# Performance work log

Measured on AMD Instinct MI355X. Metric: run time of the kernel, lower is better.

## Reference

```python
import jax, jax.numpy as jnp
import numpy as np

N_NODES = 50000
N_EDGES = 1600000
N_GRAPHS = 128
DIM_IN = 128
DIM_SELF = 16


def setup_inputs() -> dict:
    key = jax.random.key(0)
    ks = jax.random.split(key, 12)
    feat = jax.random.normal(ks[0], (N_NODES, DIM_IN), dtype=jnp.float32)
    self_feat = jax.random.normal(ks[1], (N_GRAPHS, DIM_SELF), dtype=jnp.float32)
    src = jax.random.randint(ks[2], (N_EDGES,), 0, N_NODES)
    dst = jax.random.randint(ks[3], (N_EDGES,), 0, N_NODES)
    graph_id = jnp.sort(jax.random.randint(ks[4], (N_NODES,), 0, N_GRAPHS))
    def lin(k, fan_in, fan_out):
        bound = 1.0 / np.sqrt(fan_in)
        return jax.random.uniform(k, (fan_in, fan_out), dtype=jnp.float32, minval=-bound, maxval=bound)
    W1 = lin(ks[5], DIM_IN, 100)
    b1 = jnp.zeros((100,), jnp.float32)
    W2 = lin(ks[6], 100, 20)
    b2 = jnp.zeros((20,), jnp.float32)
    Wf1 = lin(ks[7], 20 + DIM_SELF, 10)
    bf1 = jnp.zeros((10,), jnp.float32)
    Wf2 = lin(ks[8], 10, 1)
    bf2 = jnp.zeros((1,), jnp.float32)
    return {"feat": feat, "self_feat": self_feat, "src": src, "dst": dst,
            "graph_id": graph_id, "W1": W1, "b1": b1, "W2": W2, "b2": b2,
            "Wf1": Wf1, "bf1": bf1, "Wf2": Wf2, "bf2": bf2}


def _gcn_layer(h, src, dst, deg, W, b):
    # copy_u gather over edges + mean segment reduce over dst, then linear apply
    msg_sum = jax.ops.segment_sum(h[src], dst, num_segments=h.shape[0])  # [N, d]
    mean = msg_sum / jnp.maximum(deg, 1.0)[:, None]
    # DGL update_all leaves zero-in-degree nodes with their prior feature
    h_agg = jnp.where((deg > 0)[:, None], mean, h)
    return h_agg @ W + b


def reference(feat, self_feat, src, dst, graph_id, W1, b1, W2, b2, Wf1, bf1, Wf2, bf2):
    n = feat.shape[0]
    deg = jax.ops.segment_sum(jnp.ones((src.shape[0],), feat.dtype), dst, num_segments=n)
    h = jax.nn.relu(_gcn_layer(feat, src, dst, deg, W1, b1))   # [N,100]
    h = jax.nn.relu(_gcn_layer(h, src, dst, deg, W2, b2))      # [N,20]
    # dgl.mean_nodes: per-graph mean of node features
    g_sum = jax.ops.segment_sum(h, graph_id, num_segments=N_GRAPHS)  # [G,20]
    g_cnt = jax.ops.segment_sum(jnp.ones((n,), h.dtype), graph_id, num_segments=N_GRAPHS)
    hg = g_sum / jnp.maximum(g_cnt, 1.0)[:, None]
    fused = jnp.concatenate([hg, self_feat], axis=1)           # [G, 20+dim_self]
    out = jax.nn.relu(fused @ Wf1 + bf1) @ Wf2 + bf2           # [G, dim_out]
    return out
```

## Files before the change

### kernel.cpp

```cpp
#include <hip/hip_runtime.h>

constexpr int NN = 50000;
constexpr int NE = 1600000;
constexpr int NG = 128;
constexpr int BSTRIDE = 96;

constexpr int FILL_PASSES = 8;
constexpr int NODES_PER_PASS = 6250;
constexpr int BLOCKS_PER_PASS = (NE + 255) / 256;

constexpr int A1_NODES = 16;
constexpr int A1_BLOCKS = NN / A1_NODES;
constexpr int A2_BLOCKS = NN / 16;

#define OFF_CNT      0
#define OFF_GSUM     200000
#define OFF_GCNT     210240
#define ZERO_BYTES   210752
#define OFF_ADJ      210752
#define OFF_X1F      9810816
#define OFF_X2B      16210816

typedef float v2f __attribute__((ext_vector_type(2)));

__device__ __forceinline__ unsigned short f2bf(float x) {
    unsigned int v = __float_as_uint(x);
    return (unsigned short)((v + 0x7FFFu + ((v >> 16) & 1u)) >> 16);
}
__device__ __forceinline__ float bflo(unsigned int u) { return __uint_as_float(u << 16); }
__device__ __forceinline__ float bfhi(unsigned int u) { return __uint_as_float(u & 0xFFFF0000u); }

__global__ void k_fill(const int* __restrict__ src, const int* __restrict__ dst,
                       int* __restrict__ cnt, unsigned short* __restrict__ adj) {
    const int pass = blockIdx.x & 7;
    const int chunk = blockIdx.x >> 3;
    const int i = chunk * 256 + threadIdx.x;
    if (i >= NE) return;
    const int d = dst[i];
    const int lo = pass * NODES_PER_PASS;
    if (d >= lo && d < lo + NODES_PER_PASS) {
        const int p = atomicAdd(&cnt[d], 1);
        if (p < BSTRIDE) adj[d * BSTRIDE + p] = (unsigned short)src[i];
    }
}

__global__ __launch_bounds__(256) void k_gemm1(const float4* __restrict__ feat4,
                                               const float* __restrict__ W1,
                                               unsigned int* __restrict__ X1f) {
    const int t = threadIdx.x;
    if (t >= 250) return;
    const int cg = t % 25;
    const int nq = t / 25;
    const int node0 = blockIdx.x * 40 + nq * 4;
    const int col0 = cg * 4;

    float acc[4][4];
#pragma unroll
    for (int i = 0; i < 4; ++i)
#pragma unroll
        for (int j = 0; j < 4; ++j) acc[i][j] = 0.f;

    for (int k4 = 0; k4 < 32; ++k4) {
        float4 f[4];
#pragma unroll
        for (int i = 0; i < 4; ++i) f[i] = feat4[(node0 + i) * 32 + k4];
        float4 wr[4];
#pragma unroll
        for (int kk = 0; kk < 4; ++kk)
            wr[kk] = *(const float4*)(W1 + (k4 * 4 + kk) * 100 + col0);
#pragma unroll
        for (int kk = 0; kk < 4; ++kk) {
#pragma unroll
            for (int i = 0; i < 4; ++i) {
                const float fv = (kk == 0) ? f[i].x
                               : (kk == 1) ? f[i].y
                               : (kk == 2) ? f[i].z : f[i].w;
                acc[i][0] += fv * wr[kk].x;
                acc[i][1] += fv * wr[kk].y;
                acc[i][2] += fv * wr[kk].z;
                acc[i][3] += fv * wr[kk].w;
            }
        }
    }
#pragma unroll
    for (int i = 0; i < 4; ++i) {
        int u = 0;
        u = __builtin_amdgcn_cvt_pk_fp8_f32(acc[i][0], acc[i][1], u, false);
        u = __builtin_amdgcn_cvt_pk_fp8_f32(acc[i][2], acc[i][3], u, true);
        X1f[(node0 + i) * 32 + cg] = (unsigned int)u;
        if (cg == 24) {
#pragma unroll
            for (int z = 25; z < 32; ++z) X1f[(node0 + i) * 32 + z] = 0u;
        }
    }
}

__global__ __launch_bounds__(256) void k_agg1g2(
        const uint4* __restrict__ X1u, const int* __restrict__ cnt,
        const unsigned short* __restrict__ adj, const float* __restrict__ b1,
        const float* __restrict__ W2, unsigned int* __restrict__ X2b) {
    __shared__ float hl[A1_NODES * 100];
    __shared__ float w2s[100 * 20];
    const int t = threadIdx.x;
    const int node0 = blockIdx.x * A1_NODES;
    for (int i = t; i < 2000; i += 256) w2s[i] = W2[i];

    const int nl   = t >> 4;
    const int l    = t & 15;
    const int q    = l & 7;
    const int half = l >> 3;
    const int node = node0 + nl;
    const int d = cnt[node];
    const unsigned short* ab = adj + node * BSTRIDE;
    float a[16];
#pragma unroll
    for (int j = 0; j < 16; ++j) a[j] = 0.f;

#define ACC4(UU, B) { v2f l_ = __builtin_amdgcn_cvt_pk_f32_fp8((int)(UU), false); \
                      v2f h_ = __builtin_amdgcn_cvt_pk_f32_fp8((int)(UU), true);  \
                      a[B+0] += l_.x; a[B+1] += l_.y; a[B+2] += h_.x; a[B+3] += h_.y; }
#define SET4(UU, B) { v2f l_ = __builtin_amdgcn_cvt_pk_f32_fp8((int)(UU), false); \
                      v2f h_ = __builtin_amdgcn_cvt_pk_f32_fp8((int)(UU), true);  \
                      a[B+0] = l_.x; a[B+1] = l_.y; a[B+2] = h_.x; a[B+3] = h_.y; }

    if (q < 7) {
        if (d == 0) {
            if (half == 0) {
                const uint4 u = X1u[node * 8 + q];
                SET4(u.x, 0) SET4(u.y, 4) SET4(u.z, 8) SET4(u.w, 12)
            }
        } else {
            const int i0 = half ? (d >> 1) : 0;
            const int i1 = half ? d : (d >> 1);
            for (int i = i0; i < i1; ++i) {
                const int s = (int)ab[i];
                const uint4 u = X1u[s * 8 + q];
                ACC4(u.x, 0) ACC4(u.y, 4) ACC4(u.z, 8) ACC4(u.w, 12)
            }
        }
    }
#undef ACC4
#undef SET4
#pragma unroll
    for (int j = 0; j < 16; ++j) a[j] += __shfl_xor(a[j], 8);

    if (half == 0 && q < 7) {
        if (d > 0) {
            const float inv = 1.f / (float)d;
#pragma unroll
            for (int j = 0; j < 16; ++j) a[j] *= inv;
        }
        const int col0 = 16 * q;
        float* hrow = hl + nl * 100 + col0;
        const int nc = (q < 6) ? 16 : 4;
#pragma unroll 4
        for (int j = 0; j < nc; ++j)
            hrow[j] = fmaxf(a[j] + b1[col0 + j], 0.f);
    }
    __syncthreads();

    const int j = t & 15;
    unsigned int o = 0u;
    if (j < 10) {
        const float* h = hl + nl * 100;
        float a0 = 0.f, a1 = 0.f;
#pragma unroll 5
        for (int k = 0; k < 100; ++k) {
            const float hv = h[k];
            a0 += hv * w2s[k * 20 + 2 * j];
            a1 += hv * w2s[k * 20 + 2 * j + 1];
        }
        o = (unsigned int)f2bf(a0) | ((unsigned int)f2bf(a1) << 16);
    }
    X2b[node * 16 + j] = o;
}

__global__ __launch_bounds__(256) void k_agg2(const uint2* __restrict__ X2v,
                                              const int* __restrict__ cnt,
                                              const unsigned short* __restrict__ adj,
                                              const float* __restrict__ b2,
                                              const int* __restrict__ graph_id,
                                              float* __restrict__ g_sum,
                                              float* __restrict__ g_cnt) {
    __shared__ float lsum[NG * 20];
    __shared__ float lcnt[NG];
    const int t = threadIdx.x;
    for (int i = t; i < NG * 20; i += 256) lsum[i] = 0.f;
    if (t < NG) lcnt[t] = 0.f;
    __syncthreads();

    const int nl   = t >> 4;
    const int l    = t & 15;
    const int q    = l & 7;
    const int half = l >> 3;
    const int node = blockIdx.x * 16 + nl;
    const int d = cnt[node];
    const unsigned short* ab = adj + node * BSTRIDE;
    float ax = 0.f, ay = 0.f, az = 0.f, aw = 0.f;
    if (q < 5) {
        if (d == 0) {
            if (half == 0) {
                const uint2 u = X2v[node * 8 + q];
                ax = bflo(u.x); ay = bfhi(u.x);
                az = bflo(u.y); aw = bfhi(u.y);
            }
        } else {
            const int i0 = half ? (d >> 1) : 0;
            const int i1 = half ? d : (d >> 1);
            for (int i = i0; i < i1; ++i) {
                const int s = (int)ab[i];
                const uint2 u = X2v[s * 8 + q];
                ax += bflo(u.x); ay += bfhi(u.x);
                az += bflo(u.y); aw += bfhi(u.y);
            }
        }
    }
    ax += __shfl_xor(ax, 8);
    ay += __shfl_xor(ay, 8);
    az += __shfl_xor(az, 8);
    aw += __shfl_xor(aw, 8);

    if (half == 0 && q < 5) {
        if (d > 0) {
            const float inv = 1.f / (float)d;
            ax *= inv; ay *= inv; az *= inv; aw *= inv;
        }
        const int col0 = 4 * q;
        const float hx = fmaxf(ax + b2[col0 + 0], 0.f);
        const float hy = fmaxf(ay + b2[col0 + 1], 0.f);
        const float hz = fmaxf(az + b2[col0 + 2], 0.f);
        const float hw = fmaxf(aw + b2[col0 + 3], 0.f);
        const int g = graph_id[node];
        atomicAdd(&lsum[g * 20 + col0 + 0], hx);
        atomicAdd(&lsum[g * 20 + col0 + 1], hy);
        atomicAdd(&lsum[g * 20 + col0 + 2], hz);
        atomicAdd(&lsum[g * 20 + col0 + 3], hw);
    }
    if (l == 0) atomicAdd(&lcnt[graph_id[node]], 1.f);
    __syncthreads();

    const int first = blockIdx.x * 16;
    const int gmin = graph_id[first];
    const int span = graph_id[first + 15] - gmin + 1;
    for (int idx = t; idx < span * 20; idx += 256) {
        const int g = gmin + idx / 20;
        const int c = idx - (idx / 20) * 20;
        const float v = lsum[g * 20 + c];
        if (v != 0.f) atomicAdd(&g_sum[g * 20 + c], v);
    }
    for (int idx = t; idx < span; idx += 256) {
        const float v = lcnt[gmin + idx];
        if (v != 0.f) atomicAdd(&g_cnt[gmin + idx], v);
    }
}

__global__ __launch_bounds__(128) void k_final(const float* __restrict__ g_sum,
                                               const float* __restrict__ g_cnt,
                                               const float* __restrict__ self_feat,
                                               const float* __restrict__ Wf1,
                                               const float* __restrict__ bf1,
                                               const float* __restrict__ Wf2,
                                               const float* __restrict__ bf2,
                                               float* __restrict__ out) {
    const int g = threadIdx.x;
    float fused[36];
    const float cnt = fmaxf(g_cnt[g], 1.f);
    const float inv = 1.f / cnt;
#pragma unroll
    for (int j = 0; j < 20; ++j) fused[j] = g_sum[g * 20 + j] * inv;
#pragma unroll
    for (int j = 0; j < 16; ++j) fused[20 + j] = self_feat[g * 16 + j];
    float o = bf2[0];
#pragma unroll
    for (int i = 0; i < 10; ++i) {
        float t = bf1[i];
#pragma unroll
        for (int k = 0; k < 36; ++k) t += fused[k] * Wf1[k * 10 + i];
        o += fmaxf(t, 0.f) * Wf2[i];
    }
    out[g] = o;
}

extern "C" void kernel_launch(void* const* d_in, const int* in_sizes, int n_in,
                              void* d_out, int out_size, void* d_ws, size_t ws_size,
                              hipStream_t stream) {
    const float* feat      = (const float*)d_in[0];
    const float* self_feat = (const float*)d_in[1];
    const int*   src       = (const int*)d_in[2];
    const int*   dst       = (const int*)d_in[3];
    const int*   graph_id  = (const int*)d_in[4];
    const float* W1        = (const float*)d_in[5];
    const float* b1        = (const float*)d_in[6];
    const float* W2        = (const float*)d_in[7];
    const float* b2        = (const float*)d_in[8];
    const float* Wf1       = (const float*)d_in[9];
    const float* bf1       = (const float*)d_in[10];
    const float* Wf2       = (const float*)d_in[11];
    const float* bf2       = (const float*)d_in[12];

    char* w = (char*)d_ws;
    int*            cnt      = (int*)(w + OFF_CNT);
    float*          g_sum    = (float*)(w + OFF_GSUM);
    float*          g_cnt    = (float*)(w + OFF_GCNT);
    unsigned short* adj      = (unsigned short*)(w + OFF_ADJ);
    unsigned int*   X1f      = (unsigned int*)(w + OFF_X1F);
    unsigned int*   X2b      = (unsigned int*)(w + OFF_X2B);

    hipMemsetAsync(w, 0, ZERO_BYTES, stream);

    k_fill<<<FILL_PASSES * BLOCKS_PER_PASS, 256, 0, stream>>>(src, dst, cnt, adj);
    k_gemm1<<<1250, 256, 0, stream>>>((const float4*)feat, W1, X1f);
    k_agg1g2<<<A1_BLOCKS, 256, 0, stream>>>((const uint4*)X1f, cnt, adj, b1,
                                            W2, X2b);
    k_agg2<<<A2_BLOCKS, 256, 0, stream>>>((const uint2*)X2b, cnt,
                                          adj, b2, graph_id, g_sum, g_cnt);
    k_final<<<1, 128, 0, stream>>>(g_sum, g_cnt, self_feat, Wf1, bf1, Wf2, bf2,
                                   (float*)d_out);
}
```

Measured before the change: 296.0 us.

## Fuse edge bucket fill and first GEMM into one interleaved launch

Merges the adjacency fill kernel and the first dense GEMM into a single kernel, interleaving GEMM blocks among fill blocks (one GEMM super-slot every 41). The atomic-bound fill and the compute-bound GEMM are independent, so they can share the GPU concurrently, and one launch boundary is removed. The cost is more complex block indexing and register pressure set by the GEMM path for all blocks.

```diff
diff --git a/kernel.cpp b/kernel.cpp
--- a/kernel.cpp
+++ b/kernel.cpp
@@ -7,7 +7,12 @@
 
 constexpr int FILL_PASSES = 8;
 constexpr int NODES_PER_PASS = 6250;
-constexpr int BLOCKS_PER_PASS = (NE + 255) / 256;
+constexpr int FILL_CHUNKS = 6250;
+constexpr int G1_PERIOD = 41;
+constexpr int G1_SLOT = 20;
+constexpr int G1_VBLOCKS = 1250;
+constexpr int TOTAL_SUPERS = 6417;
+constexpr int FUSED_BLOCKS = TOTAL_SUPERS * 8;
 
 constexpr int A1_NODES = 16;
 constexpr int A1_BLOCKS = NN / A1_NODES;
@@ -30,28 +35,36 @@
 __device__ __forceinline__ float bflo(unsigned int u) { return __uint_as_float(u << 16); }
 __device__ __forceinline__ float bfhi(unsigned int u) { return __uint_as_float(u & 0xFFFF0000u); }
 
-__global__ void k_fill(const int* __restrict__ src, const int* __restrict__ dst,
-                       int* __restrict__ cnt, unsigned short* __restrict__ adj) {
-    const int pass = blockIdx.x & 7;
-    const int chunk = blockIdx.x >> 3;
-    const int i = chunk * 256 + threadIdx.x;
-    if (i >= NE) return;
-    const int d = dst[i];
-    const int lo = pass * NODES_PER_PASS;
-    if (d >= lo && d < lo + NODES_PER_PASS) {
-        const int p = atomicAdd(&cnt[d], 1);
-        if (p < BSTRIDE) adj[d * BSTRIDE + p] = (unsigned short)src[i];
-    }
-}
-
-__global__ __launch_bounds__(256) void k_gemm1(const float4* __restrict__ feat4,
-                                               const float* __restrict__ W1,
-                                               unsigned int* __restrict__ X1f) {
+__global__ __launch_bounds__(256) void k_fill_gemm1(
+        const int* __restrict__ src, const int* __restrict__ dst,
+        int* __restrict__ cnt, unsigned short* __restrict__ adj,
+        const float4* __restrict__ feat4, const float* __restrict__ W1,
+        unsigned int* __restrict__ X1f) {
+    const unsigned int super = blockIdx.x >> 3;
+    const unsigned int lane8 = blockIdx.x & 7;
+    const unsigned int qq = super / G1_PERIOD;
+    const unsigned int rr = super - qq * G1_PERIOD;
+
+    if (rr != G1_SLOT) {
+        const int chunk = (int)(super - qq - (rr > G1_SLOT ? 1u : 0u));
+        if (chunk >= FILL_CHUNKS) return;
+        const int i = chunk * 256 + threadIdx.x;
+        const int d = dst[i];
+        const int lo = (int)lane8 * NODES_PER_PASS;
+        if (d >= lo && d < lo + NODES_PER_PASS) {
+            const int p = atomicAdd(&cnt[d], 1);
+            if (p < BSTRIDE) adj[d * BSTRIDE + p] = (unsigned short)src[i];
+        }
+        return;
+    }
+
+    const int gb = (int)(qq * 8 + lane8);
+    if (gb >= G1_VBLOCKS) return;
     const int t = threadIdx.x;
     if (t >= 250) return;
     const int cg = t % 25;
     const int nq = t / 25;
-    const int node0 = blockIdx.x * 40 + nq * 4;
+    const int node0 = gb * 40 + nq * 4;
     const int col0 = cg * 4;
 
     float acc[4][4];
@@ -308,8 +321,8 @@
 
     hipMemsetAsync(w, 0, ZERO_BYTES, stream);
 
-    k_fill<<<FILL_PASSES * BLOCKS_PER_PASS, 256, 0, stream>>>(src, dst, cnt, adj);
-    k_gemm1<<<1250, 256, 0, stream>>>((const float4*)feat, W1, X1f);
+    k_fill_gemm1<<<FUSED_BLOCKS, 256, 0, stream>>>(src, dst, cnt, adj,
+                                                   (const float4*)feat, W1, X1f);
     k_agg1g2<<<A1_BLOCKS, 256, 0, stream>>>((const uint4*)X1f, cnt, adj, b1,
                                             W2, X2b);
     k_agg2<<<A2_BLOCKS, 256, 0, stream>>>((const uint2*)X2b, cnt,
```

New measurement: 270.4 us. 1.09x faster.
